# Optimization experiments

Measured on AMD Instinct MI355X. Metric: run time of the kernel, lower is better.

Reference implementation:

```python
import jax, jax.numpy as jnp
import numpy as np

# Model config (matches init_kwargs)
D = 2048      # model dim
H = 16        # query heads
KVH = 4       # kv heads (GQA)
HD = 128      # head dim
G = H // KVH  # groups
CAP = 50.0    # soft cap (Gemma2-style)
EPS = 1e-6
SCALE = HD ** -0.5
B, T = 2, 2048


def _rmsnorm(x, gamma):
    # RMSNorm over last dim: x / sqrt(mean(x^2)+eps) * gamma
    return x * jax.lax.rsqrt(jnp.mean(x * x, axis=-1, keepdims=True) + EPS) * gamma


def setup_inputs() -> dict:
    key = jax.random.key(0)
    ks = jax.random.split(key, 5)
    s = 0.02
    return {
        "x": jax.random.normal(ks[0], (B, T, D), dtype=jnp.float32),
        "wq": jax.random.normal(ks[1], (H * HD, D), dtype=jnp.float32) * s,
        "wk": jax.random.normal(ks[2], (KVH * HD, D), dtype=jnp.float32) * s,
        "wv": jax.random.normal(ks[3], (KVH * HD, D), dtype=jnp.float32) * s,
        "wo": jax.random.normal(ks[4], (D, H * HD), dtype=jnp.float32) * s,
        "q_gamma": jnp.ones((HD,), dtype=jnp.float32),
        "k_gamma": jnp.ones((HD,), dtype=jnp.float32),
    }


def reference(x, wq, wk, wv, wo, q_gamma, k_gamma):
    b, t, _ = x.shape
    # Projections (nn.Linear: x @ W^T), split into heads -> (b, h, t, hd)
    q = (x @ wq.T).reshape(b, t, H, HD).transpose(0, 2, 1, 3)
    k = (x @ wk.T).reshape(b, t, KVH, HD).transpose(0, 2, 1, 3)
    v = (x @ wv.T).reshape(b, t, KVH, HD).transpose(0, 2, 1, 3)
    # QK-norm (per-head-dim RMSNorm)
    q = _rmsnorm(q, q_gamma)
    k = _rmsnorm(k, k_gamma)
    # GQA: expand kv heads to match query heads (repeat_interleave on head axis)
    k = jnp.repeat(k, G, axis=1)
    v = jnp.repeat(v, G, axis=1)
    # Scores with tanh soft-cap, causal mask, softmax
    attn = jnp.einsum('bhtd,bhsd->bhts', q, k) * SCALE
    attn = CAP * jnp.tanh(attn / CAP)
    causal = jnp.triu(jnp.ones((t, t), dtype=bool), k=1)
    attn = jnp.where(causal, -jnp.inf, attn)
    attn = jax.nn.softmax(attn, axis=-1)
    out = jnp.einsum('bhts,bhsd->bhtd', attn, v)
    out = out.transpose(0, 2, 1, 3).reshape(b, t, H * HD)
    return out @ wo.T
```

## Files before the change

kernel.cpp:

```cpp
#include <hip/hip_runtime.h>

typedef __attribute__((ext_vector_type(4))) float f32x4;
typedef __attribute__((ext_vector_type(8))) short bf16x8;
typedef __attribute__((ext_vector_type(4))) unsigned short us4;
typedef unsigned short ushort_t;

__device__ __forceinline__ float bf2f(ushort_t u){
  union { unsigned int i; float f; } v; v.i = ((unsigned int)u) << 16; return v.f;
}
__device__ __forceinline__ ushort_t f2bf(float f){
  union { float f; unsigned int i; } v; v.f = f;
  unsigned int r = v.i + 0x7fffu + ((v.i >> 16) & 1u);
  return (ushort_t)(r >> 16);
}
__device__ __forceinline__ void async16(const ushort_t* g, ushort_t* l){
  __builtin_amdgcn_global_load_lds(
      (const __attribute__((address_space(1))) unsigned int*)g,
      (__attribute__((address_space(3))) unsigned int*)l, 16, 0, 0);
}

__global__ void detect_f32(const ushort_t* __restrict__ probe, int* __restrict__ flag){
  const int lane = threadIdx.x;
  int big = 0;
  for (int i = lane; i < 4096; i += 64) {
    const int ex = (probe[i] >> 7) & 0xFF;
    if (ex >= 0x90) big++;
  }
#pragma unroll
  for (int off = 32; off > 0; off >>= 1) big += __shfl_xor(big, off);
  if (lane == 0) *flag = (big > 16) ? 1 : 0;
}

__global__ __launch_bounds__(256) void convert_all(
    const void* s0, const void* s1, const void* s2, const void* s3,
    const void* s4, const void* s5, const void* s6,
    ushort_t* d0, ushort_t* d1, ushort_t* d2, ushort_t* d3,
    ushort_t* d4, ushort_t* d5, ushort_t* d6,
    const int* __restrict__ flag)
{
  long i = ((long)blockIdx.x * 256 + threadIdx.x) * 4;
  if (i >= 18874624L) return;
  const void* src; ushort_t* dst; long loc;
  if      (i <  8388608L) { src = s0; dst = d0; loc = i; }
  else if (i < 12582912L) { src = s1; dst = d1; loc = i - 8388608L; }
  else if (i < 13631488L) { src = s2; dst = d2; loc = i - 12582912L; }
  else if (i < 14680064L) { src = s3; dst = d3; loc = i - 13631488L; }
  else if (i < 18874368L) { src = s4; dst = d4; loc = i - 14680064L; }
  else if (i < 18874496L) { src = s5; dst = d5; loc = i - 18874368L; }
  else                    { src = s6; dst = d6; loc = i - 18874496L; }
  if (*flag != 0) {
    f32x4 v = *(const f32x4*)((const float*)src + loc);
    us4 o; o[0] = f2bf(v[0]); o[1] = f2bf(v[1]); o[2] = f2bf(v[2]); o[3] = f2bf(v[3]);
    *(us4*)(dst + loc) = o;
  } else {
    *(us4*)(dst + loc) = *(const us4*)((const ushort_t*)src + loc);
  }
}

#define BK 64
__global__ __launch_bounds__(256) void qkv_gemm(
    const ushort_t* __restrict__ A,
    const ushort_t* __restrict__ Wq, const ushort_t* __restrict__ Wk,
    const ushort_t* __restrict__ Wv,
    ushort_t* __restrict__ Q, ushort_t* __restrict__ Kb, ushort_t* __restrict__ Vt)
{
  __shared__ __align__(16) ushort_t As[128*BK];
  __shared__ __align__(16) ushort_t Bs[128*BK];
  const int tid = threadIdx.x;
  const int lane = tid & 63, wave = tid >> 6;
  const int quad = lane >> 4, l16 = lane & 15;
  const int m0 = blockIdx.y * 128;
  const int n0g = blockIdx.x * 128;
  const ushort_t* B; int n0, mode;
  if      (n0g < 2048) { B = Wq; n0 = n0g;        mode = 0; }
  else if (n0g < 2560) { B = Wk; n0 = n0g - 2048; mode = 1; }
  else                 { B = Wv; n0 = n0g - 2560; mode = 2; }
  const int wm = (wave >> 1) * 64, wn = (wave & 1) * 64;
  const int srow = lane >> 3, sslot = lane & 7;

  f32x4 acc[4][4];
#pragma unroll
  for (int i = 0; i < 4; i++)
#pragma unroll
    for (int j = 0; j < 4; j++) acc[i][j] = (f32x4){0.f,0.f,0.f,0.f};

  for (int k0 = 0; k0 < 2048; k0 += BK) {
    __syncthreads();
#pragma unroll
    for (int i = 0; i < 4; i++) {
      const int r0 = wave*32 + i*8;
      const int row = r0 + srow;
      const int g = (sslot ^ (row & 7)) * 8;
      async16(A + (size_t)(m0 + row)*2048 + k0 + g, &As[r0*64]);
      async16(B + (size_t)(n0 + row)*2048 + k0 + g, &Bs[r0*64]);
    }
    __syncthreads();
#pragma unroll
    for (int kc = 0; kc < 2; kc++) {
      bf16x8 af[4], bfr[4];
#pragma unroll
      for (int i = 0; i < 4; i++) {
        const int ra = wm + i*16 + l16;
        af[i] = *(const bf16x8*)&As[ra*64 + (((kc*4 + quad) ^ (ra & 7)))*8];
        const int rb = wn + i*16 + l16;
        bfr[i] = *(const bf16x8*)&Bs[rb*64 + (((kc*4 + quad) ^ (rb & 7)))*8];
      }
#pragma unroll
      for (int i = 0; i < 4; i++)
#pragma unroll
        for (int j = 0; j < 4; j++)
          acc[i][j] = __builtin_amdgcn_mfma_f32_16x16x32_bf16(af[i], bfr[j], acc[i][j], 0, 0, 0);
    }
  }
#pragma unroll
  for (int i = 0; i < 4; i++) {
    const int rbase = m0 + wm + i*16 + quad*4;
#pragma unroll
    for (int j = 0; j < 4; j++) {
      const int col = n0 + wn + j*16 + l16;
      if (mode == 0) {
#pragma unroll
        for (int r = 0; r < 4; r++) Q[(size_t)(rbase + r)*2048 + col] = f2bf(acc[i][j][r]);
      } else if (mode == 1) {
#pragma unroll
        for (int r = 0; r < 4; r++) Kb[(size_t)(rbase + r)*512 + col] = f2bf(acc[i][j][r]);
      } else {
        us4 pk;
#pragma unroll
        for (int r = 0; r < 4; r++) pk[r] = f2bf(acc[i][j][r]);
        const size_t addr = (size_t)((rbase >> 11)*512 + col)*2048 + (rbase & 2047);
        *(us4*)&Vt[addr] = pk;
      }
    }
  }
}

__global__ __launch_bounds__(256) void rmsnorm_rows(
    ushort_t* __restrict__ buf, const ushort_t* __restrict__ gamma, int nvec)
{
  const int vec = blockIdx.x * 4 + (threadIdx.x >> 6);
  const int lane = threadIdx.x & 63;
  if (vec >= nvec) return;
  const size_t base = (size_t)vec * 128 + lane*2;
  unsigned int p = *(const unsigned int*)&buf[base];
  float a = bf2f((ushort_t)(p & 0xffff));
  float b = bf2f((ushort_t)(p >> 16));
  float ss = a*a + b*b;
#pragma unroll
  for (int off = 32; off > 0; off >>= 1) ss += __shfl_xor(ss, off);
  const float sc = rsqrtf(ss * (1.0f/128.0f) + 1e-6f);
  unsigned int gp = *(const unsigned int*)&gamma[lane*2];
  float g0 = bf2f((ushort_t)(gp & 0xffff));
  float g1 = bf2f((ushort_t)(gp >> 16));
  unsigned int o = (unsigned int)f2bf(a*sc*g0) | ((unsigned int)f2bf(b*sc*g1) << 16);
  *(unsigned int*)&buf[base] = o;
}

__global__ __launch_bounds__(256) void attn_fused(
    const ushort_t* __restrict__ qbuf, const ushort_t* __restrict__ kbuf,
    const ushort_t* __restrict__ vtbuf, const ushort_t* __restrict__ qgamma,
    ushort_t* __restrict__ obuf)
{
  __shared__ __align__(16) ushort_t Ks[2][64*128];
  __shared__ __align__(16) ushort_t VTs[2][128*64];
  __shared__ __align__(16) ushort_t Ps[4][16*72];
  const int tid = threadIdx.x;
  const int lane = tid & 63, wave = tid >> 6;
  const int quad = lane >> 4, l16 = lane & 15;
  const int bx = 31 - blockIdx.x;
  const int h = blockIdx.y, b = blockIdx.z;
  const int kvh = h >> 2;
  const size_t bT = (size_t)b * 2048;
  const int qrow = bx*64 + wave*16 + l16;
  const size_t vbase = ((size_t)(b*4 + kvh)) * 128 * 2048;

  const ushort_t* qptr = qbuf + (bT + qrow)*2048 + h*128;
  float qv[4][8];
  float ss = 0.f;
#pragma unroll
  for (int kc = 0; kc < 4; kc++) {
    bf16x8 v = *(const bf16x8*)&qptr[kc*32 + quad*8];
#pragma unroll
    for (int j = 0; j < 8; j++) { float f = bf2f((ushort_t)v[j]); qv[kc][j] = f; ss += f*f; }
  }
  ss += __shfl_xor(ss, 16);
  ss += __shfl_xor(ss, 32);
  const float qsc = rsqrtf(ss*(1.0f/128.0f) + 1e-6f) * 0.08838834764831845f;
  bf16x8 qf[4];
#pragma unroll
  for (int kc = 0; kc < 4; kc++) {
    bf16x8 g = *(const bf16x8*)&qgamma[kc*32 + quad*8];
    bf16x8 o;
#pragma unroll
    for (int j = 0; j < 8; j++) o[j] = (short)f2bf(qv[kc][j] * qsc * bf2f((ushort_t)g[j]));
    qf[kc] = o;
  }

  f32x4 Ob[8];
#pragma unroll
  for (int i = 0; i < 8; i++) Ob[i] = (f32x4){0.f,0.f,0.f,0.f};
  float l_run = 0.f;

  auto stageK = [&](int kb, int bsel){
#pragma unroll
    for (int i = 0; i < 4; i++) {
      const int r0 = wave*16 + i*4;
      const int row = r0 + (lane >> 4);
      const int g = ((lane & 15) ^ (row & 15)) * 8;
      async16(kbuf + (bT + kb*64 + row)*512 + kvh*128 + g, &Ks[bsel][r0*128]);
    }
  };
  auto stageV = [&](int kb, int bsel){
#pragma unroll
    for (int i = 0; i < 4; i++) {
      const int r0 = wave*32 + i*8;
      const int d = r0 + (lane >> 3);
      const int g = ((lane & 7) ^ (d & 7)) * 8;
      async16(vtbuf + vbase + (size_t)d*2048 + kb*64 + g, &VTs[bsel][r0*64]);
    }
  };

  stageK(0, 0); stageV(0, 0);

  for (int kb = 0; kb <= bx; kb++) {
    __syncthreads();
    if (kb < bx) { stageK(kb+1, (kb+1)&1); stageV(kb+1, (kb+1)&1); }
    const int cur = kb & 1;

    f32x4 st[4];
#pragma unroll
    for (int s = 0; s < 4; s++) {
      f32x4 c = (f32x4){0.f,0.f,0.f,0.f};
#pragma unroll
      for (int kc = 0; kc < 4; kc++) {
        const int row = s*16 + l16;
        const bf16x8 kf = *(const bf16x8*)&Ks[cur][row*128 + (((kc*4 + quad) ^ (row & 15)))*8];
        c = __builtin_amdgcn_mfma_f32_16x16x32_bf16(kf, qf[kc], c, 0, 0, 0);
      }
      st[s] = c;
    }

    const bool diag = (kb == bx);
    const int myq = wave*16 + l16;
    float rsum = 0.f;
#pragma unroll
    for (int s = 0; s < 4; s++) {
      us4 pk;
#pragma unroll
      for (int r = 0; r < 4; r++) {
        const float x = st[s][r];
        const float e = __expf(x * -0.04f);
        const float t = (1.f - e) * __builtin_amdgcn_rcpf(1.f + e);
        float p = __expf(t * 50.f);
        if (diag && (s*16 + quad*4 + r) > myq) p = 0.f;
        rsum += p;
        pk[r] = f2bf(p);
      }
      *(us4*)&Ps[wave][l16*72 + s*16 + quad*4] = pk;
    }
    l_run += rsum;

#pragma unroll
    for (int kc = 0; kc < 2; kc++) {
      const bf16x8 pf = *(const bf16x8*)&Ps[wave][l16*72 + kc*32 + quad*8];
#pragma unroll
      for (int dt = 0; dt < 8; dt++) {
        const int d = dt*16 + l16;
        const bf16x8 vf = *(const bf16x8*)&VTs[cur][d*64 + (((kc*4 + quad) ^ (d & 7)))*8];
        Ob[dt] = __builtin_amdgcn_mfma_f32_16x16x32_bf16(vf, pf, Ob[dt], 0, 0, 0);
      }
    }
  }

  l_run += __shfl_xor(l_run, 16);
  l_run += __shfl_xor(l_run, 32);
  const float inv_l = __builtin_amdgcn_rcpf(l_run);
  ushort_t* optr = obuf + (bT + qrow)*2048 + h*128;
#pragma unroll
  for (int dt = 0; dt < 8; dt++) {
    us4 pk;
#pragma unroll
    for (int r = 0; r < 4; r++) pk[r] = f2bf(Ob[dt][r] * inv_l);
    *(us4*)&optr[dt*16 + quad*4] = pk;
  }
}

__global__ __launch_bounds__(256) void gemm_final(
    const ushort_t* __restrict__ A, const ushort_t* __restrict__ B,
    ushort_t* __restrict__ C, float* __restrict__ Cf, const int* __restrict__ flag)
{
  __shared__ __align__(16) ushort_t As[128*BK];
  __shared__ __align__(16) ushort_t Bs[128*BK];
  const int tid = threadIdx.x;
  const int lane = tid & 63, wave = tid >> 6;
  const int quad = lane >> 4, l16 = lane & 15;
  const int m0 = blockIdx.y * 128, n0 = blockIdx.x * 128;
  const int wm = (wave >> 1) * 64, wn = (wave & 1) * 64;
  const int srow = lane >> 3, sslot = lane & 7;

  f32x4 acc[4][4];
#pragma unroll
  for (int i = 0; i < 4; i++)
#pragma unroll
    for (int j = 0; j < 4; j++) acc[i][j] = (f32x4){0.f,0.f,0.f,0.f};

  for (int k0 = 0; k0 < 2048; k0 += BK) {
    __syncthreads();
#pragma unroll
    for (int i = 0; i < 4; i++) {
      const int r0 = wave*32 + i*8;
      const int row = r0 + srow;
      const int g = (sslot ^ (row & 7)) * 8;
      async16(A + (size_t)(m0 + row)*2048 + k0 + g, &As[r0*64]);
      async16(B + (size_t)(n0 + row)*2048 + k0 + g, &Bs[r0*64]);
    }
    __syncthreads();
#pragma unroll
    for (int kc = 0; kc < 2; kc++) {
      bf16x8 af[4], bfr[4];
#pragma unroll
      for (int i = 0; i < 4; i++) {
        const int ra = wm + i*16 + l16;
        af[i] = *(const bf16x8*)&As[ra*64 + (((kc*4 + quad) ^ (ra & 7)))*8];
        const int rb = wn + i*16 + l16;
        bfr[i] = *(const bf16x8*)&Bs[rb*64 + (((kc*4 + quad) ^ (rb & 7)))*8];
      }
#pragma unroll
      for (int i = 0; i < 4; i++)
#pragma unroll
        for (int j = 0; j < 4; j++)
          acc[i][j] = __builtin_amdgcn_mfma_f32_16x16x32_bf16(af[i], bfr[j], acc[i][j], 0, 0, 0);
    }
  }
  const bool isf = (*flag != 0);
#pragma unroll
  for (int i = 0; i < 4; i++) {
    const int rbase = m0 + wm + i*16 + quad*4;
#pragma unroll
    for (int j = 0; j < 4; j++) {
      const int col = n0 + wn + j*16 + l16;
#pragma unroll
      for (int r = 0; r < 4; r++) {
        if (isf) Cf[(size_t)(rbase + r)*2048 + col] = acc[i][j][r];
        else     C [(size_t)(rbase + r)*2048 + col] = f2bf(acc[i][j][r]);
      }
    }
  }
}

extern "C" void kernel_launch(void* const* d_in, const int* in_sizes, int n_in,
                              void* d_out, int out_size, void* d_ws, size_t ws_size,
                              hipStream_t stream)
{
  int* flag = (int*)d_ws;
  ushort_t* ws = (ushort_t*)d_ws + 8;
  ushort_t* xb  = ws;
  ushort_t* wqb = xb  + (size_t)8388608;
  ushort_t* wkb = wqb + (size_t)4194304;
  ushort_t* wvb = wkb + (size_t)1048576;
  ushort_t* wob = wvb + (size_t)1048576;
  ushort_t* qgb = wob + (size_t)4194304;
  ushort_t* kgb = qgb + 128;
  ushort_t* qbuf = kgb + 128;
  ushort_t* kbuf  = qbuf + (size_t)8388608;
  ushort_t* vtbuf = kbuf + (size_t)2097152;
  ushort_t* obuf = xb;

  detect_f32<<<1, 64, 0, stream>>>((const ushort_t*)d_in[1], flag);
  convert_all<<<18433, 256, 0, stream>>>(
      d_in[0], d_in[1], d_in[2], d_in[3], d_in[4], d_in[5], d_in[6],
      xb, wqb, wkb, wvb, wob, qgb, kgb, flag);

  qkv_gemm<<<dim3(24, 32), 256, 0, stream>>>(xb, wqb, wkb, wvb, qbuf, kbuf, vtbuf);
  rmsnorm_rows<<<dim3(4096), 256, 0, stream>>>(kbuf, kgb, 16384);
  attn_fused<<<dim3(32, 16, 2), 256, 0, stream>>>(qbuf, kbuf, vtbuf, qgb, obuf);
  gemm_final<<<dim3(16, 32), 256, 0, stream>>>(obuf, wob, (ushort_t*)d_out, (float*)d_out, flag);
}
```

Baseline: 385.6 us.

## Single-buffer attention LDS with register prefetch, polynomial softcap, vectorized K-norm

Result: no change. 391.3 us (+1.5%).

```diff
diff --git a/kernel.cpp b/kernel.cpp
--- a/kernel.cpp
+++ b/kernel.cpp
@@ -136,33 +136,33 @@
 }
 
 __global__ __launch_bounds__(256) void rmsnorm_rows(
-    ushort_t* __restrict__ buf, const ushort_t* __restrict__ gamma, int nvec)
-{
-  const int vec = blockIdx.x * 4 + (threadIdx.x >> 6);
-  const int lane = threadIdx.x & 63;
-  if (vec >= nvec) return;
-  const size_t base = (size_t)vec * 128 + lane*2;
-  unsigned int p = *(const unsigned int*)&buf[base];
-  float a = bf2f((ushort_t)(p & 0xffff));
-  float b = bf2f((ushort_t)(p >> 16));
-  float ss = a*a + b*b;
-#pragma unroll
-  for (int off = 32; off > 0; off >>= 1) ss += __shfl_xor(ss, off);
+    ushort_t* __restrict__ buf, const ushort_t* __restrict__ gamma)
+{
+  const int lane = threadIdx.x & 63, wave = threadIdx.x >> 6;
+  const int quad = lane >> 4, l16 = lane & 15;
+  const int vec = blockIdx.x*16 + wave*4 + quad;
+  const size_t base = (size_t)vec*128 + l16*8;
+  bf16x8 v = *(const bf16x8*)&buf[base];
+  float f[8]; float ss = 0.f;
+#pragma unroll
+  for (int j = 0; j < 8; j++) { f[j] = bf2f((ushort_t)v[j]); ss += f[j]*f[j]; }
+#pragma unroll
+  for (int off = 1; off < 16; off <<= 1) ss += __shfl_xor(ss, off);
   const float sc = rsqrtf(ss * (1.0f/128.0f) + 1e-6f);
-  unsigned int gp = *(const unsigned int*)&gamma[lane*2];
-  float g0 = bf2f((ushort_t)(gp & 0xffff));
-  float g1 = bf2f((ushort_t)(gp >> 16));
-  unsigned int o = (unsigned int)f2bf(a*sc*g0) | ((unsigned int)f2bf(b*sc*g1) << 16);
-  *(unsigned int*)&buf[base] = o;
-}
-
-__global__ __launch_bounds__(256) void attn_fused(
+  bf16x8 g = *(const bf16x8*)&gamma[l16*8];
+  bf16x8 o;
+#pragma unroll
+  for (int j = 0; j < 8; j++) o[j] = (short)f2bf(f[j]*sc*bf2f((ushort_t)g[j]));
+  *(bf16x8*)&buf[base] = o;
+}
+
+__global__ __launch_bounds__(256, 3) void attn_fused(
     const ushort_t* __restrict__ qbuf, const ushort_t* __restrict__ kbuf,
     const ushort_t* __restrict__ vtbuf, const ushort_t* __restrict__ qgamma,
     ushort_t* __restrict__ obuf)
 {
-  __shared__ __align__(16) ushort_t Ks[2][64*128];
-  __shared__ __align__(16) ushort_t VTs[2][128*64];
+  __shared__ __align__(16) ushort_t Ks[64*128];
+  __shared__ __align__(16) ushort_t VTs[128*64];
   __shared__ __align__(16) ushort_t Ps[4][16*72];
   const int tid = threadIdx.x;
   const int lane = tid & 63, wave = tid >> 6;
@@ -201,31 +201,37 @@
   for (int i = 0; i < 8; i++) Ob[i] = (f32x4){0.f,0.f,0.f,0.f};
   float l_run = 0.f;
 
-  auto stageK = [&](int kb, int bsel){
+  const ushort_t* kg0 = kbuf + (bT + wave*16 + (lane>>4))*512 + kvh*128;
+  const ushort_t* vg0 = vtbuf + vbase + (size_t)(wave*32 + (lane>>3))*2048;
+  bf16x8 kreg[4], vreg[4];
+  auto loadKV = [&](int kb){
 #pragma unroll
     for (int i = 0; i < 4; i++) {
-      const int r0 = wave*16 + i*4;
-      const int row = r0 + (lane >> 4);
-      const int g = ((lane & 15) ^ (row & 15)) * 8;
-      async16(kbuf + (bT + kb*64 + row)*512 + kvh*128 + g, &Ks[bsel][r0*128]);
+      const int sw = ((lane & 15) ^ ((i*4 + (lane>>4)) & 15)) * 8;
+      kreg[i] = *(const bf16x8*)(kg0 + (size_t)(kb*64 + i*4)*512 + sw);
+    }
+#pragma unroll
+    for (int i = 0; i < 4; i++) {
+      const int sw = ((lane & 7) ^ ((i*8 + (lane>>3)) & 7)) * 8;
+      vreg[i] = *(const bf16x8*)(vg0 + (size_t)(i*8)*2048 + kb*64 + sw);
     }
   };
-  auto stageV = [&](int kb, int bsel){
-#pragma unroll
-    for (int i = 0; i < 4; i++) {
-      const int r0 = wave*32 + i*8;
-      const int d = r0 + (lane >> 3);
-      const int g = ((lane & 7) ^ (d & 7)) * 8;
-      async16(vtbuf + vbase + (size_t)d*2048 + kb*64 + g, &VTs[bsel][r0*64]);
-    }
+  auto writeKV = [&](){
+#pragma unroll
+    for (int i = 0; i < 4; i++)
+      *(bf16x8*)&Ks[(wave*16 + i*4)*128 + lane*8] = kreg[i];
+#pragma unroll
+    for (int i = 0; i < 4; i++)
+      *(bf16x8*)&VTs[(wave*32 + i*8)*64 + lane*8] = vreg[i];
   };
 
-  stageK(0, 0); stageV(0, 0);
+  loadKV(0);
+  writeKV();
+  __syncthreads();
 
   for (int kb = 0; kb <= bx; kb++) {
-    __syncthreads();
-    if (kb < bx) { stageK(kb+1, (kb+1)&1); stageV(kb+1, (kb+1)&1); }
-    const int cur = kb & 1;
+    const bool last = (kb == bx);
+    if (!last) loadKV(kb+1);
 
     f32x4 st[4];
 #pragma unroll
@@ -234,13 +240,12 @@
 #pragma unroll
       for (int kc = 0; kc < 4; kc++) {
         const int row = s*16 + l16;
-        const bf16x8 kf = *(const bf16x8*)&Ks[cur][row*128 + (((kc*4 + quad) ^ (row & 15)))*8];
+        const bf16x8 kf = *(const bf16x8*)&Ks[row*128 + (((kc*4 + quad) ^ (row & 15)))*8];
         c = __builtin_amdgcn_mfma_f32_16x16x32_bf16(kf, qf[kc], c, 0, 0, 0);
       }
       st[s] = c;
     }
 
-    const bool diag = (kb == bx);
     const int myq = wave*16 + l16;
     float rsum = 0.f;
 #pragma unroll
@@ -249,10 +254,11 @@
 #pragma unroll
       for (int r = 0; r < 4; r++) {
         const float x = st[s][r];
-        const float e = __expf(x * -0.04f);
-        const float t = (1.f - e) * __builtin_amdgcn_rcpf(1.f + e);
-        float p = __expf(t * 50.f);
-        if (diag && (s*16 + quad*4 + r) > myq) p = 0.f;
+        const float w = x*x;
+        const float t2 = x * __builtin_fmaf(w,
+            __builtin_fmaf(w, 3.0777494e-8f, -1.9235934e-4f), 1.4426950408889634f);
+        float p = __builtin_amdgcn_exp2f(t2);
+        if (last && (s*16 + quad*4 + r) > myq) p = 0.f;
         rsum += p;
         pk[r] = f2bf(p);
       }
@@ -266,9 +272,16 @@
 #pragma unroll
       for (int dt = 0; dt < 8; dt++) {
         const int d = dt*16 + l16;
-        const bf16x8 vf = *(const bf16x8*)&VTs[cur][d*64 + (((kc*4 + quad) ^ (d & 7)))*8];
+        const bf16x8 vf = *(const bf16x8*)&VTs[d*64 + (((kc*4 + quad) ^ (d & 7)))*8];
         Ob[dt] = __builtin_amdgcn_mfma_f32_16x16x32_bf16(vf, pf, Ob[dt], 0, 0, 0);
       }
+    }
+
+    if (!last) {
+      __builtin_amdgcn_s_waitcnt(0xC07F);
+      __builtin_amdgcn_s_barrier();
+      writeKV();
+      __syncthreads();
     }
   }
 
@@ -372,7 +385,7 @@
       xb, wqb, wkb, wvb, wob, qgb, kgb, flag);
 
   qkv_gemm<<<dim3(24, 32), 256, 0, stream>>>(xb, wqb, wkb, wvb, qbuf, kbuf, vtbuf);
-  rmsnorm_rows<<<dim3(4096), 256, 0, stream>>>(kbuf, kgb, 16384);
+  rmsnorm_rows<<<dim3(1024), 256, 0, stream>>>(kbuf, kgb);
   attn_fused<<<dim3(32, 16, 2), 256, 0, stream>>>(qbuf, kbuf, vtbuf, qgb, obuf);
   gemm_final<<<dim3(16, 32), 256, 0, stream>>>(obuf, wob, (ushort_t*)d_out, (float*)d_out, flag);
 }
```
